# Kernel optimization log

Hardware: AMD Instinct MI355X
Metric: run time of the kernel (lower is better)

## Reference

```python
import jax, jax.numpy as jnp
import numpy as np

E = 8                 # n_experts
CAPACITY_FACTOR = 1.25

B, T, H, I = 4, 1024, 2048, 1408


def setup_inputs() -> dict:
    key = jax.random.key(0)
    k0, k1, k2, k3, k4 = jax.random.split(key, 5)
    x = jax.random.normal(k0, (B, T, H), jnp.float32)
    Wr = jax.random.normal(k1, (E, H), jnp.float32) * 0.02   # router proj (no bias)
    Wg = jax.random.normal(k2, (E, I, H), jnp.float32) * 0.02  # gate_proj per expert
    Wu = jax.random.normal(k3, (E, I, H), jnp.float32) * 0.02  # up_proj per expert
    Wd = jax.random.normal(k4, (E, H, I), jnp.float32) * 0.02  # down_proj per expert
    return {"x": x, "Wr": Wr, "Wg": Wg, "Wu": Wu, "Wd": Wd}


def reference(x, Wr, Wg, Wu, Wd):
    Bb, Tt, Hh = x.shape
    N = Bb * Tt
    cap = max(1, int(CAPACITY_FACTOR * (N * 2 / E)))
    xf = x.reshape(N, Hh)

    # --- Top2Router (noise_std=0 -> no noise) ---
    logits = jnp.einsum('nh,eh->ne', xf, Wr)          # [N, E]
    gate = jax.nn.softmax(logits, axis=-1)
    top2_val, top2_idx = jax.lax.top_k(gate, 2)        # [N, 2]

    # --- capacity masking, matching torch loop order: slot k=0 over all
    # tokens (flat order), then slot k=1; within an expert the first `cap`
    # assignments are kept ---
    flat_idx = jnp.concatenate([top2_idx[:, 0], top2_idx[:, 1]])   # [2N]
    flat_val = jnp.concatenate([top2_val[:, 0], top2_val[:, 1]])   # [2N]
    onehot = jax.nn.one_hot(flat_idx, E, dtype=jnp.int32)          # [2N, E]
    rank = (jnp.cumsum(onehot, axis=0) * onehot).sum(-1)           # inclusive rank within expert
    keep = rank <= cap                                             # [2N]
    w_assign = jnp.where(keep, flat_val, 0.0)

    # combine weights per (token, expert); top-2 experts per token are distinct
    tok = jnp.tile(jnp.arange(N), 2)
    comb = jnp.zeros((N, E), x.dtype).at[tok, flat_idx].add(w_assign)  # [N, E]

    # --- per-expert SwiGLU FFN applied densely, combined with gate weights ---
    g = jax.nn.silu(jnp.einsum('nh,eih->eni', xf, Wg))  # [E, N, I]
    u = jnp.einsum('nh,eih->eni', xf, Wu)               # [E, N, I]
    out_e = jnp.einsum('eni,ehi->enh', g * u, Wd)       # [E, N, H]
    y = jnp.einsum('ne,enh->nh', comb, out_e)           # [N, H]
    return y.reshape(Bb, Tt, Hh)
```

## Files before the change

### kernel.cpp

```cpp
#include <hip/hip_runtime.h>
#include <hip/hip_bf16.h>

#define N_TOK 4096
#define H_DIM 2048
#define I_DIM 1408
#define E_NUM 8
#define CAP   1280

typedef __hip_bfloat16 bf16;
typedef unsigned short us;
typedef __bf16 bf16x8 __attribute__((ext_vector_type(8)));
typedef float f32x4 __attribute__((ext_vector_type(4)));

__device__ inline void gld_lds16(const void* g, void* l) {
    __builtin_amdgcn_global_load_lds((const __attribute__((address_space(1))) void*)g,
                                     (__attribute__((address_space(3))) void*)l,
                                     16, 0, 0);
}

__device__ inline void cvt_body8(const float* __restrict__ s, us* __restrict__ d, long i, long n) {
    if (i >= n) return;
    float4 v0 = *(const float4*)(s + i);
    float4 v1 = *(const float4*)(s + i + 4);
    union { us u[8]; uint4 q; } o;
    float f[8] = {v0.x, v0.y, v0.z, v0.w, v1.x, v1.y, v1.z, v1.w};
#pragma unroll
    for (int j = 0; j < 8; j++) {
        bf16 b = __float2bfloat16(f[j]);
        o.u[j] = *(us*)&b;
    }
    *(uint4*)(d + i) = o.q;
}

__global__ void cvt8(const float* __restrict__ s, us* __restrict__ d, long n) {
    long i = ((long)blockIdx.x * blockDim.x + threadIdx.x) * 8;
    cvt_body8(s, d, i, n);
}

__global__ void cvt_w3(const float* __restrict__ s0, const float* __restrict__ s1,
                       const float* __restrict__ s2, us* __restrict__ d0,
                       us* __restrict__ d1, us* __restrict__ d2, long n) {
    long i = ((long)blockIdx.x * blockDim.x + threadIdx.x) * 8;
    const float* s = blockIdx.z == 0 ? s0 : (blockIdx.z == 1 ? s1 : s2);
    us* d = blockIdx.z == 0 ? d0 : (blockIdx.z == 1 ? d1 : d2);
    cvt_body8(s, d, i, n);
}

__global__ void router_k(const float* __restrict__ x, const float* __restrict__ Wr,
                         float* __restrict__ top_val, int* __restrict__ top_idx) {
    int tok  = (blockIdx.x * blockDim.x + threadIdx.x) >> 6;
    int lane = threadIdx.x & 63;
    if (tok >= N_TOK) return;
    const float* xr = x + (size_t)tok * H_DIM;
    float acc[E_NUM];
#pragma unroll
    for (int e = 0; e < E_NUM; e++) acc[e] = 0.f;
    for (int h = lane; h < H_DIM; h += 64) {
        float xv = xr[h];
#pragma unroll
        for (int e = 0; e < E_NUM; e++) acc[e] += xv * Wr[e * H_DIM + h];
    }
#pragma unroll
    for (int e = 0; e < E_NUM; e++) {
#pragma unroll
        for (int off = 32; off > 0; off >>= 1) acc[e] += __shfl_xor(acc[e], off, 64);
    }
    if (lane == 0) {
        float mx = acc[0];
#pragma unroll
        for (int e = 1; e < E_NUM; e++) mx = fmaxf(mx, acc[e]);
        float p[E_NUM], s = 0.f;
#pragma unroll
        for (int e = 0; e < E_NUM; e++) { p[e] = __expf(acc[e] - mx); s += p[e]; }
        float inv = 1.f / s;
#pragma unroll
        for (int e = 0; e < E_NUM; e++) p[e] *= inv;
        int i0 = 0;
#pragma unroll
        for (int e = 1; e < E_NUM; e++) if (p[e] > p[i0]) i0 = e;
        int i1 = -1;
#pragma unroll
        for (int e = 0; e < E_NUM; e++) {
            if (e == i0) continue;
            if (i1 < 0 || p[e] > p[i1]) i1 = e;
        }
        top_idx[tok * 2]     = i0;
        top_idx[tok * 2 + 1] = i1;
        top_val[tok * 2]     = p[i0];
        top_val[tok * 2 + 1] = p[i1];
    }
}

__global__ void assign_k(const int* __restrict__ top_idx, const float* __restrict__ top_val,
                         int* __restrict__ toklist, float* __restrict__ wlist,
                         int* __restrict__ counts) {
    const int T = 256;
    const int CH = (2 * N_TOK) / T;
    int t = threadIdx.x;
    for (int i = t; i < E_NUM * CAP; i += T) { toklist[i] = N_TOK; wlist[i] = 0.f; }
    __shared__ int cnt[T][E_NUM];
    int local[E_NUM];
#pragma unroll
    for (int e = 0; e < E_NUM; e++) local[e] = 0;
    for (int q = 0; q < CH; q++) {
        int j = t * CH + q;
        int slot = j >> 12;
        int tok  = j & 4095;
        int e = top_idx[tok * 2 + slot];
        local[e]++;
    }
#pragma unroll
    for (int e = 0; e < E_NUM; e++) cnt[t][e] = local[e];
    __syncthreads();
    if (t < E_NUM) {
        int run = 0;
        for (int i = 0; i < T; i++) { int c = cnt[i][t]; cnt[i][t] = run; run += c; }
        counts[t] = run < CAP ? run : CAP;
    }
    __syncthreads();
    int run[E_NUM];
#pragma unroll
    for (int e = 0; e < E_NUM; e++) run[e] = cnt[t][e];
    for (int q = 0; q < CH; q++) {
        int j = t * CH + q;
        int slot = j >> 12;
        int tok  = j & 4095;
        int e = top_idx[tok * 2 + slot];
        int rank = ++run[e];
        if (rank <= CAP) {
            toklist[e * CAP + rank - 1] = tok;
            wlist[e * CAP + rank - 1]   = top_val[tok * 2 + slot];
        }
    }
}

__global__ __launch_bounds__(256, 3)
void gu_gemm(const us* __restrict__ A, const us* __restrict__ Wg,
             const us* __restrict__ Wu, us* __restrict__ gbuf, us* __restrict__ ubuf,
             const int* __restrict__ toklist, const int* __restrict__ counts) {
    const int z  = blockIdx.z;
    const int e  = z & 7;
    const int isU = z >> 3;
    const int m0 = blockIdx.x * 128;
    const int n0 = blockIdx.y * 128;
    if (m0 >= counts[e]) return;

    const us* W = isU ? Wu : Wg;
    us* obuf    = isU ? ubuf : gbuf;

    __shared__ us As[128 * 64];
    __shared__ us Bs[128 * 64];

    const int t  = threadIdx.x;
    const int r0 = t >> 2;
    const int c8 = (t & 3) * 8;

    int tok0 = toklist[e * CAP + m0 + r0];
    int tok1 = toklist[e * CAP + m0 + r0 + 64];
    const us* aP0 = A + (size_t)tok0 * H_DIM + c8;
    const us* aP1 = A + (size_t)tok1 * H_DIM + c8;
    const us* bP0 = W + ((size_t)e * I_DIM + n0 + r0) * H_DIM + c8;
    const us* bP1 = bP0 + (size_t)64 * H_DIM;

    us* lA0 = As + t * 8;  us* lA1 = lA0 + 64 * 32;
    us* lB0 = Bs + t * 8;  us* lB1 = lB0 + 64 * 32;

    const int lane = t & 63;
    const int wave = t >> 6;
    const int wm   = (wave & 1) * 64;
    const int wn   = (wave >> 1) * 64;
    const int l15  = lane & 15;
    const int quad = lane >> 4;

    f32x4 acc[4][4];
#pragma unroll
    for (int i = 0; i < 4; i++)
#pragma unroll
        for (int j = 0; j < 4; j++) acc[i][j] = (f32x4){0.f, 0.f, 0.f, 0.f};

    for (int k = 0; k < H_DIM; k += 64) {
        gld_lds16(aP0,      lA0);
        gld_lds16(aP1,      lA1);
        gld_lds16(aP0 + 32, lA0 + 4096);
        gld_lds16(aP1 + 32, lA1 + 4096);
        gld_lds16(bP0,      lB0);
        gld_lds16(bP1,      lB1);
        gld_lds16(bP0 + 32, lB0 + 4096);
        gld_lds16(bP1 + 32, lB1 + 4096);
        aP0 += 64; aP1 += 64; bP0 += 64; bP1 += 64;
        __syncthreads();
#pragma unroll
        for (int kk = 0; kk < 2; kk++) {
            bf16x8 af[4], bfr[4];
#pragma unroll
            for (int i = 0; i < 4; i++)
                af[i] = *(const bf16x8*)(As + kk * 4096 + (wm + i * 16 + l15) * 32 + quad * 8);
#pragma unroll
            for (int j = 0; j < 4; j++)
                bfr[j] = *(const bf16x8*)(Bs + kk * 4096 + (wn + j * 16 + l15) * 32 + quad * 8);
#pragma unroll
            for (int i = 0; i < 4; i++)
#pragma unroll
                for (int j = 0; j < 4; j++)
                    acc[i][j] = __builtin_amdgcn_mfma_f32_16x16x32_bf16(af[i], bfr[j], acc[i][j], 0, 0, 0);
        }
        __syncthreads();
    }

#pragma unroll
    for (int i = 0; i < 4; i++) {
        int mb = m0 + wm + i * 16 + quad * 4;
#pragma unroll
        for (int r = 0; r < 4; r++) {
            size_t rowoff = ((size_t)e * CAP + mb + r) * I_DIM;
#pragma unroll
            for (int j = 0; j < 4; j++) {
                int n = n0 + wn + j * 16 + l15;
                float v = acc[i][j][r];
                if (!isU) v = v / (1.f + __expf(-v));
                bf16 b = __float2bfloat16(v);
                obuf[rowoff + n] = *(us*)&b;
            }
        }
    }
}

__global__ void swiglu_mul(const us* __restrict__ g, const us* __restrict__ u,
                           us* __restrict__ h, long n) {
    long i = ((long)blockIdx.x * blockDim.x + threadIdx.x) * 8;
    if (i >= n) return;
    uint4 gq = *(const uint4*)(g + i);
    uint4 uq = *(const uint4*)(u + i);
    const us* gp = (const us*)&gq;
    const us* up = (const us*)&uq;
    union { us u[8]; uint4 q; } o;
#pragma unroll
    for (int j = 0; j < 8; j++) {
        float gv = __bfloat162float(*(const bf16*)&gp[j]);
        float uv = __bfloat162float(*(const bf16*)&up[j]);
        bf16 b = __float2bfloat16(gv * uv);
        o.u[j] = *(us*)&b;
    }
    *(uint4*)(h + i) = o.q;
}

__global__ __launch_bounds__(256, 3)
void down_gemm(const us* __restrict__ A, const us* __restrict__ W,
               float* __restrict__ out,
               const int* __restrict__ toklist, const float* __restrict__ wlist,
               const int* __restrict__ counts) {
    const int z  = blockIdx.z;
    const int e  = z & 7;
    const int k0 = (z >> 3) * (I_DIM / 2);
    const int m0 = blockIdx.x * 128;
    const int n0 = blockIdx.y * 128;
    if (m0 >= counts[e]) return;

    __shared__ us As[128 * 64];
    __shared__ us Bs[128 * 64];

    const int t  = threadIdx.x;
    const int r0 = t >> 2;
    const int c8 = (t & 3) * 8;

    const us* aP0 = A + ((size_t)e * CAP + m0 + r0) * (size_t)I_DIM + k0 + c8;
    const us* aP1 = aP0 + (size_t)64 * I_DIM;
    const us* bP0 = W + ((size_t)e * H_DIM + n0 + r0) * (size_t)I_DIM + k0 + c8;
    const us* bP1 = bP0 + (size_t)64 * I_DIM;

    us* lA0 = As + t * 8;  us* lA1 = lA0 + 64 * 32;
    us* lB0 = Bs + t * 8;  us* lB1 = lB0 + 64 * 32;

    const int lane = t & 63;
    const int wave = t >> 6;
    const int wm   = (wave & 1) * 64;
    const int wn   = (wave >> 1) * 64;
    const int l15  = lane & 15;
    const int quad = lane >> 4;

    f32x4 acc[4][4];
#pragma unroll
    for (int i = 0; i < 4; i++)
#pragma unroll
        for (int j = 0; j < 4; j++) acc[i][j] = (f32x4){0.f, 0.f, 0.f, 0.f};

    for (int k = 0; k < I_DIM / 2; k += 64) {
        gld_lds16(aP0,      lA0);
        gld_lds16(aP1,      lA1);
        gld_lds16(aP0 + 32, lA0 + 4096);
        gld_lds16(aP1 + 32, lA1 + 4096);
        gld_lds16(bP0,      lB0);
        gld_lds16(bP1,      lB1);
        gld_lds16(bP0 + 32, lB0 + 4096);
        gld_lds16(bP1 + 32, lB1 + 4096);
        aP0 += 64; aP1 += 64; bP0 += 64; bP1 += 64;
        __syncthreads();
#pragma unroll
        for (int kk = 0; kk < 2; kk++) {
            bf16x8 af[4], bfr[4];
#pragma unroll
            for (int i = 0; i < 4; i++)
                af[i] = *(const bf16x8*)(As + kk * 4096 + (wm + i * 16 + l15) * 32 + quad * 8);
#pragma unroll
            for (int j = 0; j < 4; j++)
                bfr[j] = *(const bf16x8*)(Bs + kk * 4096 + (wn + j * 16 + l15) * 32 + quad * 8);
#pragma unroll
            for (int i = 0; i < 4; i++)
#pragma unroll
                for (int j = 0; j < 4; j++)
                    acc[i][j] = __builtin_amdgcn_mfma_f32_16x16x32_bf16(af[i], bfr[j], acc[i][j], 0, 0, 0);
        }
        __syncthreads();
    }

#pragma unroll
    for (int i = 0; i < 4; i++) {
        int mb = m0 + wm + i * 16 + quad * 4;
#pragma unroll
        for (int r = 0; r < 4; r++) {
            int tok = toklist[e * CAP + mb + r];
            if (tok < N_TOK) {
                float wgt = wlist[e * CAP + mb + r];
                float* orow = out + (size_t)tok * H_DIM + n0 + wn + l15;
#pragma unroll
                for (int j = 0; j < 4; j++)
                    atomicAdd(orow + j * 16, wgt * acc[i][j][r]);
            }
        }
    }
}

extern "C" void kernel_launch(void* const* d_in, const int* in_sizes, int n_in,
                              void* d_out, int out_size, void* d_ws, size_t ws_size,
                              hipStream_t stream) {
    const float* x  = (const float*)d_in[0];
    const float* Wr = (const float*)d_in[1];
    const float* Wg = (const float*)d_in[2];
    const float* Wu = (const float*)d_in[3];
    const float* Wd = (const float*)d_in[4];
    float* out = (float*)d_out;

    char* p = (char*)d_ws;
    auto alloc = [&](size_t bytes) { char* r = p; p += (bytes + 255) & ~(size_t)255; return r; };
    us* xb   = (us*)alloc((size_t)(N_TOK + 1) * H_DIM * 2);
    us* Wgb  = (us*)alloc((size_t)E_NUM * I_DIM * H_DIM * 2);
    us* Wub  = (us*)alloc((size_t)E_NUM * I_DIM * H_DIM * 2);
    us* Wdb  = (us*)alloc((size_t)E_NUM * H_DIM * I_DIM * 2);
    us* gbuf = (us*)alloc((size_t)E_NUM * CAP * I_DIM * 2);
    us* ubuf = (us*)alloc((size_t)E_NUM * CAP * I_DIM * 2);
    us* hbuf = (us*)alloc((size_t)E_NUM * CAP * I_DIM * 2);
    float* top_val = (float*)alloc((size_t)N_TOK * 2 * 4);
    int*   top_idx = (int*)alloc((size_t)N_TOK * 2 * 4);
    int*   toklist = (int*)alloc((size_t)E_NUM * CAP * 4);
    float* wlist   = (float*)alloc((size_t)E_NUM * CAP * 4);
    int*   counts  = (int*)alloc((size_t)E_NUM * 4);

    hipMemsetAsync(out, 0, (size_t)N_TOK * H_DIM * 4, stream);
    hipMemsetAsync(xb + (size_t)N_TOK * H_DIM, 0, H_DIM * 2, stream);

    long nx = (long)N_TOK * H_DIM;
    long nw = (long)E_NUM * I_DIM * H_DIM;
    cvt8<<<dim3((unsigned)((nx / 8 + 255) / 256)), dim3(256), 0, stream>>>(x, xb, nx);
    cvt_w3<<<dim3((unsigned)((nw / 8 + 255) / 256), 1, 3), dim3(256), 0, stream>>>(
        Wg, Wu, Wd, Wgb, Wub, Wdb, nw);

    router_k<<<dim3(N_TOK / 4), dim3(256), 0, stream>>>(x, Wr, top_val, top_idx);
    assign_k<<<dim3(1), dim3(256), 0, stream>>>(top_idx, top_val, toklist, wlist, counts);

    dim3 g1(CAP / 128, I_DIM / 128, 16);
    gu_gemm<<<g1, dim3(256), 0, stream>>>(xb, Wgb, Wub, gbuf, ubuf, toklist, counts);

    long nh = (long)E_NUM * CAP * I_DIM;
    swiglu_mul<<<dim3((unsigned)((nh / 8 + 255) / 256)), dim3(256), 0, stream>>>(gbuf, ubuf, hbuf, nh);

    dim3 g2(CAP / 128, H_DIM / 128, 16);
    down_gemm<<<g2, dim3(256), 0, stream>>>(hbuf, Wdb, out, toklist, wlist, counts);
}
```

Measured before the change: 688.4 us.

## Fuse gate/up GEMMs with SwiGLU and replace atomic scatter with gather combine

Gate and up projections are computed in one kernel that shares the A tile and applies SiLU*up in the epilogue, removing the separate g/u buffers and the swiglu_mul pass. The down GEMM no longer splits K or scatters with float atomics. It writes per-slot results to a dense buffer (aliased onto the converted Wg buffer), and a new combine kernel gathers each token's two expert rows and weights them. This also drops the output memset. The costs are higher register and LDS use in the fused kernel (launch bounds lowered to 2), fewer down-GEMM blocks, and an extra fp32 write and read of the per-slot results.

```diff
diff --git a/kernel.cpp b/kernel.cpp
--- a/kernel.cpp
+++ b/kernel.cpp
@@ -92,12 +92,12 @@
 }
 
 __global__ void assign_k(const int* __restrict__ top_idx, const float* __restrict__ top_val,
-                         int* __restrict__ toklist, float* __restrict__ wlist,
-                         int* __restrict__ counts) {
+                         int* __restrict__ toklist, int* __restrict__ pos,
+                         float* __restrict__ wz, int* __restrict__ counts) {
     const int T = 256;
     const int CH = (2 * N_TOK) / T;
     int t = threadIdx.x;
-    for (int i = t; i < E_NUM * CAP; i += T) { toklist[i] = N_TOK; wlist[i] = 0.f; }
+    for (int i = t; i < E_NUM * CAP; i += T) toklist[i] = N_TOK;
     __shared__ int cnt[T][E_NUM];
     int local[E_NUM];
 #pragma unroll
@@ -129,27 +129,27 @@
         int rank = ++run[e];
         if (rank <= CAP) {
             toklist[e * CAP + rank - 1] = tok;
-            wlist[e * CAP + rank - 1]   = top_val[tok * 2 + slot];
-        }
-    }
-}
-
-__global__ __launch_bounds__(256, 3)
-void gu_gemm(const us* __restrict__ A, const us* __restrict__ Wg,
-             const us* __restrict__ Wu, us* __restrict__ gbuf, us* __restrict__ ubuf,
-             const int* __restrict__ toklist, const int* __restrict__ counts) {
-    const int z  = blockIdx.z;
-    const int e  = z & 7;
-    const int isU = z >> 3;
+            pos[tok * 2 + slot] = e * CAP + rank - 1;
+            wz[tok * 2 + slot]  = top_val[tok * 2 + slot];
+        } else {
+            pos[tok * 2 + slot] = -1;
+            wz[tok * 2 + slot]  = 0.f;
+        }
+    }
+}
+
+__global__ __launch_bounds__(256, 2)
+void gu_fused(const us* __restrict__ A, const us* __restrict__ Wg,
+              const us* __restrict__ Wu, us* __restrict__ hbuf,
+              const int* __restrict__ toklist, const int* __restrict__ counts) {
+    const int e  = blockIdx.z;
     const int m0 = blockIdx.x * 128;
     const int n0 = blockIdx.y * 128;
     if (m0 >= counts[e]) return;
 
-    const us* W = isU ? Wu : Wg;
-    us* obuf    = isU ? ubuf : gbuf;
-
     __shared__ us As[128 * 64];
-    __shared__ us Bs[128 * 64];
+    __shared__ us Bg[128 * 64];
+    __shared__ us Bu[128 * 64];
 
     const int t  = threadIdx.x;
     const int r0 = t >> 2;
@@ -159,11 +159,14 @@
     int tok1 = toklist[e * CAP + m0 + r0 + 64];
     const us* aP0 = A + (size_t)tok0 * H_DIM + c8;
     const us* aP1 = A + (size_t)tok1 * H_DIM + c8;
-    const us* bP0 = W + ((size_t)e * I_DIM + n0 + r0) * H_DIM + c8;
-    const us* bP1 = bP0 + (size_t)64 * H_DIM;
+    const us* gP0 = Wg + ((size_t)e * I_DIM + n0 + r0) * H_DIM + c8;
+    const us* gP1 = gP0 + (size_t)64 * H_DIM;
+    const us* uP0 = Wu + ((size_t)e * I_DIM + n0 + r0) * H_DIM + c8;
+    const us* uP1 = uP0 + (size_t)64 * H_DIM;
 
     us* lA0 = As + t * 8;  us* lA1 = lA0 + 64 * 32;
-    us* lB0 = Bs + t * 8;  us* lB1 = lB0 + 64 * 32;
+    us* lG0 = Bg + t * 8;  us* lG1 = lG0 + 64 * 32;
+    us* lU0 = Bu + t * 8;  us* lU1 = lU0 + 64 * 32;
 
     const int lane = t & 63;
     const int wave = t >> 6;
@@ -172,13 +175,118 @@
     const int l15  = lane & 15;
     const int quad = lane >> 4;
 
+    f32x4 ag[4][4], au[4][4];
+#pragma unroll
+    for (int i = 0; i < 4; i++)
+#pragma unroll
+        for (int j = 0; j < 4; j++) {
+            ag[i][j] = (f32x4){0.f, 0.f, 0.f, 0.f};
+            au[i][j] = (f32x4){0.f, 0.f, 0.f, 0.f};
+        }
+
+    for (int k = 0; k < H_DIM; k += 64) {
+        gld_lds16(aP0,      lA0);
+        gld_lds16(aP1,      lA1);
+        gld_lds16(aP0 + 32, lA0 + 4096);
+        gld_lds16(aP1 + 32, lA1 + 4096);
+        gld_lds16(gP0,      lG0);
+        gld_lds16(gP1,      lG1);
+        gld_lds16(gP0 + 32, lG0 + 4096);
+        gld_lds16(gP1 + 32, lG1 + 4096);
+        gld_lds16(uP0,      lU0);
+        gld_lds16(uP1,      lU1);
+        gld_lds16(uP0 + 32, lU0 + 4096);
+        gld_lds16(uP1 + 32, lU1 + 4096);
+        aP0 += 64; aP1 += 64; gP0 += 64; gP1 += 64; uP0 += 64; uP1 += 64;
+        __syncthreads();
+#pragma unroll
+        for (int kk = 0; kk < 2; kk++) {
+            bf16x8 af[4];
+#pragma unroll
+            for (int i = 0; i < 4; i++)
+                af[i] = *(const bf16x8*)(As + kk * 4096 + (wm + i * 16 + l15) * 32 + quad * 8);
+            {
+                bf16x8 bfr[4];
+#pragma unroll
+                for (int j = 0; j < 4; j++)
+                    bfr[j] = *(const bf16x8*)(Bg + kk * 4096 + (wn + j * 16 + l15) * 32 + quad * 8);
+#pragma unroll
+                for (int i = 0; i < 4; i++)
+#pragma unroll
+                    for (int j = 0; j < 4; j++)
+                        ag[i][j] = __builtin_amdgcn_mfma_f32_16x16x32_bf16(af[i], bfr[j], ag[i][j], 0, 0, 0);
+            }
+            {
+                bf16x8 bfr[4];
+#pragma unroll
+                for (int j = 0; j < 4; j++)
+                    bfr[j] = *(const bf16x8*)(Bu + kk * 4096 + (wn + j * 16 + l15) * 32 + quad * 8);
+#pragma unroll
+                for (int i = 0; i < 4; i++)
+#pragma unroll
+                    for (int j = 0; j < 4; j++)
+                        au[i][j] = __builtin_amdgcn_mfma_f32_16x16x32_bf16(af[i], bfr[j], au[i][j], 0, 0, 0);
+            }
+        }
+        __syncthreads();
+    }
+
+#pragma unroll
+    for (int i = 0; i < 4; i++) {
+        int mb = m0 + wm + i * 16 + quad * 4;
+#pragma unroll
+        for (int r = 0; r < 4; r++) {
+            size_t rowoff = ((size_t)e * CAP + mb + r) * I_DIM;
+#pragma unroll
+            for (int j = 0; j < 4; j++) {
+                int n = n0 + wn + j * 16 + l15;
+                float g = ag[i][j][r];
+                g = g / (1.f + __expf(-g));
+                float hv = g * au[i][j][r];
+                bf16 b = __float2bfloat16(hv);
+                hbuf[rowoff + n] = *(us*)&b;
+            }
+        }
+    }
+}
+
+__global__ __launch_bounds__(256, 3)
+void down_gemm(const us* __restrict__ A, const us* __restrict__ W,
+               float* __restrict__ dbuf, const int* __restrict__ counts) {
+    const int e  = blockIdx.z;
+    const int m0 = blockIdx.x * 128;
+    const int n0 = blockIdx.y * 128;
+    if (m0 >= counts[e]) return;
+
+    __shared__ us As[128 * 64];
+    __shared__ us Bs[128 * 64];
+
+    const int t  = threadIdx.x;
+    const int r0 = t >> 2;
+    const int c8 = (t & 3) * 8;
+
+    const us* aP0 = A + ((size_t)e * CAP + m0 + r0) * (size_t)I_DIM + c8;
+    const us* aP1 = aP0 + (size_t)64 * I_DIM;
+    const us* bP0 = W + ((size_t)e * H_DIM + n0 + r0) * (size_t)I_DIM + c8;
+    const us* bP1 = bP0 + (size_t)64 * I_DIM;
+
+    us* lA0 = As + t * 8;  us* lA1 = lA0 + 64 * 32;
+    us* lB0 = Bs + t * 8;  us* lB1 = lB0 + 64 * 32;
+
+    const int lane = t & 63;
+    const int wave = t >> 6;
+    const int wm   = (wave & 1) * 64;
+    const int wn   = (wave >> 1) * 64;
+    const int l15  = lane & 15;
+    const int quad = lane >> 4;
+
     f32x4 acc[4][4];
 #pragma unroll
     for (int i = 0; i < 4; i++)
 #pragma unroll
         for (int j = 0; j < 4; j++) acc[i][j] = (f32x4){0.f, 0.f, 0.f, 0.f};
 
-    for (int k = 0; k < H_DIM; k += 64) {
+    for (int k = 0; k < I_DIM; k += 64) {
         gld_lds16(aP0,      lA0);
         gld_lds16(aP1,      lA1);
         gld_lds16(aP0 + 32, lA0 + 4096);
@@ -212,122 +320,38 @@
         int mb = m0 + wm + i * 16 + quad * 4;
 #pragma unroll
         for (int r = 0; r < 4; r++) {
-            size_t rowoff = ((size_t)e * CAP + mb + r) * I_DIM;
-#pragma unroll
-            for (int j = 0; j < 4; j++) {
-                int n = n0 + wn + j * 16 + l15;
-                float v = acc[i][j][r];
-                if (!isU) v = v / (1.f + __expf(-v));
-                bf16 b = __float2bfloat16(v);
-                obuf[rowoff + n] = *(us*)&b;
-            }
-        }
-    }
-}
-
-__global__ void swiglu_mul(const us* __restrict__ g, const us* __restrict__ u,
-                           us* __restrict__ h, long n) {
-    long i = ((long)blockIdx.x * blockDim.x + threadIdx.x) * 8;
-    if (i >= n) return;
-    uint4 gq = *(const uint4*)(g + i);
-    uint4 uq = *(const uint4*)(u + i);
-    const us* gp = (const us*)&gq;
-    const us* up = (const us*)&uq;
-    union { us u[8]; uint4 q; } o;
-#pragma unroll
-    for (int j = 0; j < 8; j++) {
-        float gv = __bfloat162float(*(const bf16*)&gp[j]);
-        float uv = __bfloat162float(*(const bf16*)&up[j]);
-        bf16 b = __float2bfloat16(gv * uv);
-        o.u[j] = *(us*)&b;
-    }
-    *(uint4*)(h + i) = o.q;
-}
-
-__global__ __launch_bounds__(256, 3)
-void down_gemm(const us* __restrict__ A, const us* __restrict__ W,
-               float* __restrict__ out,
-               const int* __restrict__ toklist, const float* __restrict__ wlist,
-               const int* __restrict__ counts) {
-    const int z  = blockIdx.z;
-    const int e  = z & 7;
-    const int k0 = (z >> 3) * (I_DIM / 2);
-    const int m0 = blockIdx.x * 128;
-    const int n0 = blockIdx.y * 128;
-    if (m0 >= counts[e]) return;
-
-    __shared__ us As[128 * 64];
-    __shared__ us Bs[128 * 64];
-
-    const int t  = threadIdx.x;
-    const int r0 = t >> 2;
-    const int c8 = (t & 3) * 8;
-
-    const us* aP0 = A + ((size_t)e * CAP + m0 + r0) * (size_t)I_DIM + k0 + c8;
-    const us* aP1 = aP0 + (size_t)64 * I_DIM;
-    const us* bP0 = W + ((size_t)e * H_DIM + n0 + r0) * (size_t)I_DIM + k0 + c8;
-    const us* bP1 = bP0 + (size_t)64 * I_DIM;
-
-    us* lA0 = As + t * 8;  us* lA1 = lA0 + 64 * 32;
-    us* lB0 = Bs + t * 8;  us* lB1 = lB0 + 64 * 32;
-
-    const int lane = t & 63;
-    const int wave = t >> 6;
-    const int wm   = (wave & 1) * 64;
-    const int wn   = (wave >> 1) * 64;
-    const int l15  = lane & 15;
-    const int quad = lane >> 4;
-
-    f32x4 acc[4][4];
-#pragma unroll
-    for (int i = 0; i < 4; i++)
-#pragma unroll
-        for (int j = 0; j < 4; j++) acc[i][j] = (f32x4){0.f, 0.f, 0.f, 0.f};
-
-    for (int k = 0; k < I_DIM / 2; k += 64) {
-        gld_lds16(aP0,      lA0);
-        gld_lds16(aP1,      lA1);
-        gld_lds16(aP0 + 32, lA0 + 4096);
-        gld_lds16(aP1 + 32, lA1 + 4096);
-        gld_lds16(bP0,      lB0);
-        gld_lds16(bP1,      lB1);
-        gld_lds16(bP0 + 32, lB0 + 4096);
-        gld_lds16(bP1 + 32, lB1 + 4096);
-        aP0 += 64; aP1 += 64; bP0 += 64; bP1 += 64;
-        __syncthreads();
-#pragma unroll
-        for (int kk = 0; kk < 2; kk++) {
-            bf16x8 af[4], bfr[4];
-#pragma unroll
-            for (int i = 0; i < 4; i++)
-                af[i] = *(const bf16x8*)(As + kk * 4096 + (wm + i * 16 + l15) * 32 + quad * 8);
+            float* orow = dbuf + ((size_t)e * CAP + mb + r) * H_DIM + n0 + wn + l15;
 #pragma unroll
             for (int j = 0; j < 4; j++)
-                bfr[j] = *(const bf16x8*)(Bs + kk * 4096 + (wn + j * 16 + l15) * 32 + quad * 8);
-#pragma unroll
-            for (int i = 0; i < 4; i++)
-#pragma unroll
-                for (int j = 0; j < 4; j++)
-                    acc[i][j] = __builtin_amdgcn_mfma_f32_16x16x32_bf16(af[i], bfr[j], acc[i][j], 0, 0, 0);
-        }
-        __syncthreads();
-    }
-
-#pragma unroll
-    for (int i = 0; i < 4; i++) {
-        int mb = m0 + wm + i * 16 + quad * 4;
-#pragma unroll
-        for (int r = 0; r < 4; r++) {
-            int tok = toklist[e * CAP + mb + r];
-            if (tok < N_TOK) {
-                float wgt = wlist[e * CAP + mb + r];
-                float* orow = out + (size_t)tok * H_DIM + n0 + wn + l15;
-#pragma unroll
-                for (int j = 0; j < 4; j++)
-                    atomicAdd(orow + j * 16, wgt * acc[i][j][r]);
-            }
-        }
-    }
+                orow[j * 16] = acc[i][j][r];
+        }
+    }
+}
+
+__global__ void combine_k(const float* __restrict__ dbuf, const int* __restrict__ pos,
+                          const float* __restrict__ wz, float* __restrict__ out) {
+    int tok = blockIdx.x;
+    int off = threadIdx.x * 8;
+    int p0 = pos[tok * 2], p1 = pos[tok * 2 + 1];
+    float w0 = wz[tok * 2], w1 = wz[tok * 2 + 1];
+    float4 z = {0.f, 0.f, 0.f, 0.f};
+    float4 a0 = z, a1 = z, b0 = z, b1 = z;
+    if (p0 >= 0) {
+        const float* r = dbuf + (size_t)p0 * H_DIM + off;
+        a0 = *(const float4*)r; a1 = *(const float4*)(r + 4);
+    }
+    if (p1 >= 0) {
+        const float* r = dbuf + (size_t)p1 * H_DIM + off;
+        b0 = *(const float4*)r; b1 = *(const float4*)(r + 4);
+    }
+    float4 o0, o1;
+    o0.x = w0 * a0.x + w1 * b0.x;  o0.y = w0 * a0.y + w1 * b0.y;
+    o0.z = w0 * a0.z + w1 * b0.z;  o0.w = w0 * a0.w + w1 * b0.w;
+    o1.x = w0 * a1.x + w1 * b1.x;  o1.y = w0 * a1.y + w1 * b1.y;
+    o1.z = w0 * a1.z + w1 * b1.z;  o1.w = w0 * a1.w + w1 * b1.w;
+    float* orow = out + (size_t)tok * H_DIM + off;
+    *(float4*)orow = o0;
+    *(float4*)(orow + 4) = o1;
 }
 
 extern "C" void kernel_launch(void* const* d_in, const int* in_sizes, int n_in,
@@ -346,16 +370,15 @@
     us* Wgb  = (us*)alloc((size_t)E_NUM * I_DIM * H_DIM * 2);
     us* Wub  = (us*)alloc((size_t)E_NUM * I_DIM * H_DIM * 2);
     us* Wdb  = (us*)alloc((size_t)E_NUM * H_DIM * I_DIM * 2);
-    us* gbuf = (us*)alloc((size_t)E_NUM * CAP * I_DIM * 2);
-    us* ubuf = (us*)alloc((size_t)E_NUM * CAP * I_DIM * 2);
     us* hbuf = (us*)alloc((size_t)E_NUM * CAP * I_DIM * 2);
     float* top_val = (float*)alloc((size_t)N_TOK * 2 * 4);
     int*   top_idx = (int*)alloc((size_t)N_TOK * 2 * 4);
     int*   toklist = (int*)alloc((size_t)E_NUM * CAP * 4);
-    float* wlist   = (float*)alloc((size_t)E_NUM * CAP * 4);
+    int*   posm    = (int*)alloc((size_t)N_TOK * 2 * 4);
+    float* wz      = (float*)alloc((size_t)N_TOK * 2 * 4);
     int*   counts  = (int*)alloc((size_t)E_NUM * 4);
-
-    hipMemsetAsync(out, 0, (size_t)N_TOK * H_DIM * 4, stream);
+    float* dbuf = (float*)Wgb;
+
     hipMemsetAsync(xb + (size_t)N_TOK * H_DIM, 0, H_DIM * 2, stream);
 
     long nx = (long)N_TOK * H_DIM;
@@ -365,14 +388,13 @@
         Wg, Wu, Wd, Wgb, Wub, Wdb, nw);
 
     router_k<<<dim3(N_TOK / 4), dim3(256), 0, stream>>>(x, Wr, top_val, top_idx);
-    assign_k<<<dim3(1), dim3(256), 0, stream>>>(top_idx, top_val, toklist, wlist, counts);
-
-    dim3 g1(CAP / 128, I_DIM / 128, 16);
-    gu_gemm<<<g1, dim3(256), 0, stream>>>(xb, Wgb, Wub, gbuf, ubuf, toklist, counts);
-
-    long nh = (long)E_NUM * CAP * I_DIM;
-    swiglu_mul<<<dim3((unsigned)((nh / 8 + 255) / 256)), dim3(256), 0, stream>>>(gbuf, ubuf, hbuf, nh);
-
-    dim3 g2(CAP / 128, H_DIM / 128, 16);
-    down_gemm<<<g2, dim3(256), 0, stream>>>(hbuf, Wdb, out, toklist, wlist, counts);
-}
+    assign_k<<<dim3(1), dim3(256), 0, stream>>>(top_idx, top_val, toklist, posm, wz, counts);
+
+    dim3 g1(CAP / 128, I_DIM / 128, E_NUM);
+    gu_fused<<<g1, dim3(256), 0, stream>>>(xb, Wgb, Wub, hbuf, toklist, counts);
+
+    dim3 g2(CAP / 128, H_DIM / 128, E_NUM);
+    down_gemm<<<g2, dim3(256), 0, stream>>>(hbuf, Wdb, dbuf, counts);
+
+    combine_k<<<dim3(N_TOK), dim3(256), 0, stream>>>(dbuf, posm, wz, out);
+}
```

Result: faster. 607.5 us (-11.8%).
